# Performance work log

Measured on AMD Instinct MI355X. Metric: run time of the kernel, lower is better.

## Reference

```python
import jax, jax.numpy as jnp
import numpy as np

N_EMBD = 512
BLOCK = 512
HEADS = 16
HEAD_DIM = N_EMBD // HEADS
EPS = 1e-5


def _layernorm(x, g, b):
    mu = jnp.mean(x, axis=-1, keepdims=True)
    var = jnp.mean(jnp.square(x - mu), axis=-1, keepdims=True)
    return (x - mu) * jax.lax.rsqrt(var + EPS) * g + b


def setup_inputs() -> dict:
    key = jax.random.key(0)
    ks = jax.random.split(key, 12)
    B, T, C, H, D = 64, BLOCK, N_EMBD, HEADS, HEAD_DIM
    s = lambda fan_in: 1.0 / np.sqrt(fan_in)
    return {
        "x": jax.random.normal(ks[0], (B, T, C), dtype=jnp.float32),
        # per-head projections, stored (H, C, D) so y = einsum('btc,hcd->bhtd')
        "Wq": jax.random.normal(ks[1], (H, C, D), dtype=jnp.float32) * s(C),
        "Wk": jax.random.normal(ks[2], (H, C, D), dtype=jnp.float32) * s(C),
        "Wv": jax.random.normal(ks[3], (H, C, D), dtype=jnp.float32) * s(C),
        "Wp": jax.random.normal(ks[4], (C, C), dtype=jnp.float32) * s(C),
        "bp": jnp.zeros((C,), dtype=jnp.float32),
        "W1": jax.random.normal(ks[5], (C, 4 * C), dtype=jnp.float32) * s(C),
        "b1": jnp.zeros((4 * C,), dtype=jnp.float32),
        "W2": jax.random.normal(ks[6], (4 * C, C), dtype=jnp.float32) * s(4 * C),
        "b2": jnp.zeros((C,), dtype=jnp.float32),
        "g_ln1": jnp.ones((C,), dtype=jnp.float32),
        "b_ln1": jnp.zeros((C,), dtype=jnp.float32),
        "g_ln2": jnp.ones((C,), dtype=jnp.float32),
        "b_ln2": jnp.zeros((C,), dtype=jnp.float32),
    }


def reference(x, Wq, Wk, Wv, Wp, bp, W1, b1, W2, b2, g_ln1, b_ln1, g_ln2, b_ln2):
    B, T, C = x.shape
    h = _layernorm(x, g_ln1, b_ln1)
    q = jnp.einsum('btc,hcd->bhtd', h, Wq)
    k = jnp.einsum('btc,hcd->bhtd', h, Wk)
    v = jnp.einsum('btc,hcd->bhtd', h, Wv)
    wei = jnp.einsum('bhtd,bhsd->bhts', q, k) * (HEAD_DIM ** -0.5)
    causal = jnp.tril(jnp.ones((T, T), dtype=bool))
    wei = jnp.where(causal, wei, -jnp.inf)
    wei = jax.nn.softmax(wei, axis=-1)  # dropout = identity (eval mode)
    out = jnp.einsum('bhts,bhsd->bhtd', wei, v)
    out = out.transpose(0, 2, 1, 3).reshape(B, T, C)  # concat heads
    sa = out @ Wp + bp
    x = x + sa
    h2 = _layernorm(x, g_ln2, b_ln2)
    ff = jax.nn.relu(h2 @ W1 + b1) @ W2 + b2
    return x + ff
```

## Files before the change

kernel.cpp:

```cpp
#include <hip/hip_runtime.h>
#include <stdint.h>


typedef __attribute__((ext_vector_type(8))) short bf16x8;
typedef __attribute__((ext_vector_type(4))) short bf16x4;
typedef __attribute__((ext_vector_type(4))) float f32x4;

__device__ __forceinline__ unsigned short f2bf(float x) {
  union { float f; unsigned u; } v; v.f = x;
  unsigned r = v.u + 0x7fff + ((v.u >> 16) & 1);
  return (unsigned short)(r >> 16);
}

#if __has_builtin(__builtin_amdgcn_exp2f)
__device__ __forceinline__ float exp2fast(float x) { return __builtin_amdgcn_exp2f(x); }
#else
__device__ __forceinline__ float exp2fast(float x) { return exp2f(x); }
#endif

__device__ __forceinline__ unsigned cvtpk(float lo, float hi) {
  unsigned r; asm("v_cvt_pk_bf16_f32 %0, %1, %2" : "=v"(r) : "v"(lo), "v"(hi)); return r;
}

__device__ __forceinline__ f32x4 MFMA32(bf16x8 a, bf16x8 b, f32x4 c) {
  return __builtin_amdgcn_mfma_f32_16x16x32_bf16(a, b, c, 0, 0, 0);
}

#if __has_builtin(__builtin_amdgcn_mfma_f32_16x16x16bf16_1k)
__device__ __forceinline__ f32x4 MFMA16(bf16x4 a, bf16x4 b, f32x4 c) {
  return __builtin_amdgcn_mfma_f32_16x16x16bf16_1k(a, b, c, 0, 0, 0);
}
#else
__device__ __forceinline__ f32x4 MFMA16(bf16x4 a, bf16x4 b, f32x4 c) {
  f32x4 d;
  asm volatile("v_mfma_f32_16x16x16_bf16 %0, %1, %2, %3\n\ts_nop 7\n\ts_nop 3"
               : "=v"(d) : "v"(a), "v"(b), "v"(c));
  return d;
}
#endif

__device__ __forceinline__ void gload_lds16(const void* g, void* l) {
  __builtin_amdgcn_global_load_lds(
      (const __attribute__((address_space(1))) unsigned int*)(uintptr_t)g,
      (__attribute__((address_space(3))) unsigned int*)(unsigned)(uintptr_t)l,
      16, 0, 0);
}

#define WAITV8() do { asm volatile("s_waitcnt vmcnt(8)" ::: "memory"); } while (0)
#define WAITV0() do { asm volatile("s_waitcnt vmcnt(0)" ::: "memory"); } while (0)
#define WAITL0() do { asm volatile("s_waitcnt lgkmcnt(0)" ::: "memory"); } while (0)
#define SBAR()   __builtin_amdgcn_s_barrier()
#define SCHED0() __builtin_amdgcn_sched_barrier(0)

__global__ __launch_bounds__(256) void prep_qkv_w(
    const float* __restrict__ Wq, const float* __restrict__ Wk,
    const float* __restrict__ Wv, unsigned short* __restrict__ dst)
{
  int idx = blockIdx.x * 256 + threadIdx.x;
  int k = idx & 511;
  int n = idx >> 9;
  int q = n >> 9;
  int hh = (n >> 5) & 15;
  int d = n & 31;
  const float* W = (q == 0) ? Wq : ((q == 1) ? Wk : Wv);
  dst[idx] = f2bf(W[((size_t)hh * 512 + k) * 32 + d]);
}

__global__ __launch_bounds__(256) void transpose_cast(
    const float* __restrict__ src, unsigned short* __restrict__ dst, int Kd, int Nd)
{
  int idx = blockIdx.x * 256 + threadIdx.x;
  int n = idx / Kd, k = idx - n * Kd;
  dst[idx] = f2bf(src[(size_t)k * Nd + n]);
}

__global__ __launch_bounds__(256) void ln_kernel(
    const float* __restrict__ x, const float* __restrict__ g,
    const float* __restrict__ b, unsigned short* __restrict__ out)
{
  const int lane = threadIdx.x & 63;
  const size_t row = (size_t)blockIdx.x * 4 + (threadIdx.x >> 6);
  const float* xp = x + row * 512 + lane * 8;
  float xv[8] __attribute__((aligned(16)));
  *(float4*)(xv)     = *(const float4*)(xp);
  *(float4*)(xv + 4) = *(const float4*)(xp + 4);
  float s = 0.f, s2 = 0.f;
#pragma unroll
  for (int j = 0; j < 8; ++j) { s += xv[j]; s2 += xv[j] * xv[j]; }
#pragma unroll
  for (int m = 1; m < 64; m <<= 1) { s += __shfl_xor(s, m); s2 += __shfl_xor(s2, m); }
  float mean = s * (1.f / 512.f);
  float rstd = rsqrtf(fmaxf(s2 * (1.f / 512.f) - mean * mean, 0.f) + 1e-5f);
  float gv[8] __attribute__((aligned(16))), bv[8] __attribute__((aligned(16)));
  *(float4*)(gv)     = *(const float4*)(g + lane * 8);
  *(float4*)(gv + 4) = *(const float4*)(g + lane * 8 + 4);
  *(float4*)(bv)     = *(const float4*)(b + lane * 8);
  *(float4*)(bv + 4) = *(const float4*)(b + lane * 8 + 4);
  bf16x8 o;
#pragma unroll
  for (int j = 0; j < 8; ++j) o[j] = (short)f2bf((xv[j] - mean) * rstd * gv[j] + bv[j]);
  *(bf16x8*)(out + row * 512 + lane * 8) = o;
}

__global__ __launch_bounds__(256) void vt_kernel(
    const unsigned short* __restrict__ vnat, unsigned short* __restrict__ vt)
{
  __shared__ unsigned short tile[64 * 36];
  const int bh = blockIdx.x >> 3, tt = (blockIdx.x & 7) << 6;
  const int tid = threadIdx.x;
  const int rr = tid >> 2, ch = tid & 3;
  bf16x8 v = *(const bf16x8*)(vnat + ((size_t)bh * 512 + tt + rr) * 32 + ch * 8);
  unsigned short* dst = &tile[rr * 36 + ch * 8];
#pragma unroll
  for (int j = 0; j < 8; ++j) dst[j] = (unsigned short)v[j];
  __syncthreads();
  const int d = tid >> 3, toct = (tid & 7) << 3;
  union { unsigned short s[8]; bf16x8 v8; } o;
#pragma unroll
  for (int j = 0; j < 8; ++j) o.s[j] = tile[(toct + j) * 36 + d];
  *(bf16x8*)(vt + ((size_t)bh * 32 + d) * 512 + tt + toct) = o.v8;
}

template <int MODE>
__device__ __forceinline__ void gemm256_body(
    const unsigned short* __restrict__ A, const unsigned short* __restrict__ Bt,
    int N, int K, int nby,
    unsigned short* __restrict__ obf, float* __restrict__ of32,
    const float* __restrict__ bias, const float* __restrict__ resid,
    unsigned short* __restrict__ vout)
{
  __shared__ __align__(16) unsigned short As[2][256 * 64];
  __shared__ __align__(16) unsigned short Bs[2][256 * 64];
  const int tid = threadIdx.x, lane = tid & 63, wid = tid >> 6;
  const int wr = wid >> 2, wc = wid & 3;
  const int r = lane & 15, hq = lane >> 4;

  const int qq = gridDim.x >> 3;
  const int swz = (blockIdx.x & 7) * qq + (blockIdx.x >> 3);
  const int bx = swz / nby, by = swz - bx * nby;
  const int brow = bx * 256, bcol = by * 256;
  const int nkt = K >> 6;

  const int srow = wid * 32 + (lane >> 3);
  const int schunk = ((lane & 7) ^ ((lane >> 3) & 7)) * 8;
  const unsigned short* Asrc = A + (size_t)(brow + srow) * K + schunk;
  const unsigned short* Bsrc = Bt + (size_t)(bcol + srow) * K + schunk;

  auto STAGE = [&](int t, int buf) {
    const unsigned short* as_ = Asrc + t * 64;
    const unsigned short* bs_ = Bsrc + t * 64;
    char* al_ = (char*)(&As[buf][0]) + wid * 4096;
    char* bl_ = (char*)(&Bs[buf][0]) + wid * 4096;
#pragma unroll
    for (int g = 0; g < 4; ++g) {
      gload_lds16(as_ + (size_t)g * 8 * K, al_ + g * 1024);
      gload_lds16(bs_ + (size_t)g * 8 * K, bl_ + g * 1024);
    }
  };

  const int x0 = ((hq) ^ (r & 7)) * 16;
  const int x1 = ((4 + hq) ^ (r & 7)) * 16;
  const int abase = (wr * 128 + r) * 128;
  const int bbase = (wc * 64 + r) * 128;

  f32x4 acc[8][4] = {};
  bf16x8 af[4][2], bfa[2][2], bfb[2][2];

  STAGE(0, 0);
  STAGE(1, 1);
  WAITV8(); SCHED0();
  SBAR();

  for (int t = 0; t < nkt; ++t) {
    const char* Ab = (const char*)(&As[t & 1][0]);
    const char* Bb = (const char*)(&Bs[t & 1][0]);
#pragma unroll
    for (int m = 0; m < 4; ++m) {
      af[m][0] = *(const bf16x8*)(Ab + abase + m * 2048 + x0);
      af[m][1] = *(const bf16x8*)(Ab + abase + m * 2048 + x1);
    }
#pragma unroll
    for (int n = 0; n < 2; ++n) {
      bfa[n][0] = *(const bf16x8*)(Bb + bbase + n * 2048 + x0);
      bfa[n][1] = *(const bf16x8*)(Bb + bbase + n * 2048 + x1);
    }
    SBAR();
    WAITL0(); SCHED0();
    __builtin_amdgcn_s_setprio(1);
#pragma unroll
    for (int m = 0; m < 4; ++m)
#pragma unroll
      for (int n = 0; n < 2; ++n) {
        acc[m][n] = MFMA32(af[m][0], bfa[n][0], acc[m][n]);
        acc[m][n] = MFMA32(af[m][1], bfa[n][1], acc[m][n]);
      }
    __builtin_amdgcn_s_setprio(0);
    SBAR();
#pragma unroll
    for (int n = 0; n < 2; ++n) {
      bfb[n][0] = *(const bf16x8*)(Bb + bbase + (n + 2) * 2048 + x0);
      bfb[n][1] = *(const bf16x8*)(Bb + bbase + (n + 2) * 2048 + x1);
    }
    SBAR();
    WAITL0(); SCHED0();
    __builtin_amdgcn_s_setprio(1);
#pragma unroll
    for (int m = 0; m < 4; ++m)
#pragma unroll
      for (int n = 0; n < 2; ++n) {
        acc[m][n + 2] = MFMA32(af[m][0], bfb[n][0], acc[m][n + 2]);
        acc[m][n + 2] = MFMA32(af[m][1], bfb[n][1], acc[m][n + 2]);
      }
    __builtin_amdgcn_s_setprio(0);
    SBAR();
#pragma unroll
    for (int m = 0; m < 4; ++m) {
      af[m][0] = *(const bf16x8*)(Ab + abase + 8192 + m * 2048 + x0);
      af[m][1] = *(const bf16x8*)(Ab + abase + 8192 + m * 2048 + x1);
    }
    SBAR();
    WAITL0(); SCHED0();
    __builtin_amdgcn_s_setprio(1);
#pragma unroll
    for (int m = 0; m < 4; ++m)
#pragma unroll
      for (int n = 0; n < 2; ++n) {
        acc[4 + m][n] = MFMA32(af[m][0], bfa[n][0], acc[4 + m][n]);
        acc[4 + m][n] = MFMA32(af[m][1], bfa[n][1], acc[4 + m][n]);
      }
    __builtin_amdgcn_s_setprio(0);
    SBAR();
    if (t + 2 < nkt) STAGE(t + 2, t & 1);
    __builtin_amdgcn_s_setprio(1);
#pragma unroll
    for (int m = 0; m < 4; ++m)
#pragma unroll
      for (int n = 0; n < 2; ++n) {
        acc[4 + m][n + 2] = MFMA32(af[m][0], bfb[n][0], acc[4 + m][n + 2]);
        acc[4 + m][n + 2] = MFMA32(af[m][1], bfb[n][1], acc[4 + m][n + 2]);
      }
    __builtin_amdgcn_s_setprio(0);
    if (t + 2 < nkt) { WAITV8(); } else { WAITV0(); }
    SCHED0();
    SBAR();
  }

#pragma unroll
  for (int m = 0; m < 8; ++m)
#pragma unroll
    for (int n = 0; n < 4; ++n) {
      const int row0 = brow + wr * 128 + m * 16 + hq * 4;
      const int col = bcol + wc * 64 + n * 16 + r;
#pragma unroll
      for (int q2 = 0; q2 < 4; ++q2) {
        const int row = row0 + q2;
        float v = acc[m][n][q2];
        if (MODE == 1) {
          const int which = col >> 9, hh = (col >> 5) & 15, dd = col & 31;
          const int bb = row >> 9, tt = row & 511;
          const size_t off = ((((size_t)bb) * 16 + hh) * 512 + tt) * 32 + dd;
          if (which < 2) {
            if (which == 0) v *= 0.25503521f;
            obf[(size_t)which * 16777216 + off] = f2bf(v);
          } else
            vout[off] = f2bf(v);
        } else if (MODE == 2) {
          v += bias[col] + resid[(size_t)row * N + col];
          of32[(size_t)row * N + col] = v;
        } else if (MODE == 3) {
          v = fmaxf(v + bias[col], 0.f);
          obf[(size_t)row * N + col] = f2bf(v);
        }
      }
    }
}

__global__ __launch_bounds__(512, 2) void qkv_gemm(
    const unsigned short* __restrict__ A, const unsigned short* __restrict__ Bt,
    int N, int K, int nby, unsigned short* __restrict__ obf,
    unsigned short* __restrict__ vout)
{ gemm256_body<1>(A, Bt, N, K, nby, obf, nullptr, nullptr, nullptr, vout); }

__global__ __launch_bounds__(512, 2) void proj_gemm(
    const unsigned short* __restrict__ A, const unsigned short* __restrict__ Bt,
    int N, int K, int nby, float* __restrict__ of32,
    const float* __restrict__ bias, const float* __restrict__ resid)
{ gemm256_body<2>(A, Bt, N, K, nby, nullptr, of32, bias, resid, nullptr); }

__global__ __launch_bounds__(512, 2) void ffn1_gemm(
    const unsigned short* __restrict__ A, const unsigned short* __restrict__ Bt,
    int N, int K, int nby, unsigned short* __restrict__ obf,
    const float* __restrict__ bias)
{ gemm256_body<3>(A, Bt, N, K, nby, obf, nullptr, bias, nullptr, nullptr); }

__global__ __launch_bounds__(512, 2) void ffn2_gemm(
    const unsigned short* __restrict__ A, const unsigned short* __restrict__ Bt,
    int N, int K, int nby, float* __restrict__ of32,
    const float* __restrict__ bias, const float* __restrict__ resid)
{ gemm256_body<2>(A, Bt, N, K, nby, nullptr, of32, bias, resid, nullptr); }

__global__ __launch_bounds__(512, 4) void attn_kernel(
    const unsigned short* __restrict__ Qb, const unsigned short* __restrict__ Kb,
    const unsigned short* __restrict__ Vt, unsigned short* __restrict__ att)
{
  __shared__ __align__(16) unsigned short Ks[512 * 32];
  __shared__ __align__(16) unsigned short Vs[32 * 512];
  const int tid = threadIdx.x, lane = tid & 63, wid = tid >> 6;
  const int bh = blockIdx.x;
  const int r = lane & 15, hq = lane >> 4;
  const unsigned short* Kg = Kb + (size_t)bh * (512 * 32);
  const unsigned short* Vg = Vt + (size_t)bh * (32 * 512);
#pragma unroll
  for (int it = 0; it < 4; ++it) {
    const int c = it * 512 + tid;
    gload_lds16(Kg + c * 8, (char*)Ks + (it * 512 + wid * 64) * 16);
    const int d = c >> 6, sb = c & 63;
    gload_lds16(Vg + d * 512 + (sb ^ (d & 15)) * 8, (char*)Vs + (it * 512 + wid * 64) * 16);
  }
  __syncthreads();

  const f32x4 z = {0.f, 0.f, 0.f, 0.f};
  for (int p = 0; p < 4; ++p) {
    const int t0 = (((p >> 1) << 4) + ((p & 1) ? 15 - wid : wid)) << 4;
    const bf16x8 qf = *(const bf16x8*)(Qb + ((size_t)bh * 512 + t0 + r) * 32 + hq * 8);
    f32x4 o0 = z, o1 = z;
    float m = -1e30f, l = 0.f;
    const int s0m = t0 & ~31;
    for (int s0 = 0; s0 <= s0m; s0 += 32) {
      f32x4 st0 = MFMA32(*(const bf16x8*)((const char*)Ks + (s0 + r) * 64 + hq * 16), qf, z);
      f32x4 st1 = MFMA32(*(const bf16x8*)((const char*)Ks + (s0 + 16 + r) * 64 + hq * 16), qf, z);
      if (s0 == s0m) {
        const int qq = t0 + r;
#pragma unroll
        for (int j = 0; j < 4; ++j) {
          if (s0 + 4 * hq + j > qq)      st0[j] = -1e30f;
          if (s0 + 16 + 4 * hq + j > qq) st1[j] = -1e30f;
        }
      }
      float mx = fmaxf(fmaxf(fmaxf(st0[0], st0[1]), fmaxf(st0[2], st0[3])),
                       fmaxf(fmaxf(st1[0], st1[1]), fmaxf(st1[2], st1[3])));
      mx = fmaxf(mx, __shfl_xor(mx, 16));
      mx = fmaxf(mx, __shfl_xor(mx, 32));
      if (!__all(mx <= m + 8.f)) {
        const float mn = fmaxf(m, mx);
        const float f = exp2fast(m - mn);
        m = mn; l *= f; o0 *= f; o1 *= f;
      }
      float p0[4], p1[4];
#pragma unroll
      for (int j = 0; j < 4; ++j) {
        p0[j] = exp2fast(st0[j] - m);
        p1[j] = exp2fast(st1[j] - m);
      }
      float rs = ((p0[0] + p0[1]) + (p0[2] + p0[3])) + ((p1[0] + p1[1]) + (p1[2] + p1[3]));
      rs += __shfl_xor(rs, 16);
      rs += __shfl_xor(rs, 32);
      l += rs;
      union { unsigned u[2]; bf16x4 v; } a0, a1;
      a0.u[0] = cvtpk(p0[0], p0[1]); a0.u[1] = cvtpk(p0[2], p0[3]);
      a1.u[0] = cvtpk(p1[0], p1[1]); a1.u[1] = cvtpk(p1[2], p1[3]);
      const int lb = (s0 >> 3) + (hq >> 1);
      const char* vb = (const char*)Vs + (hq & 1) * 8;
      o0 = MFMA16(a0.v, *(const bf16x4*)(vb + r * 1024 + ((lb) ^ r) * 16), o0);
      o0 = MFMA16(a1.v, *(const bf16x4*)(vb + r * 1024 + ((lb + 2) ^ r) * 16), o0);
      o1 = MFMA16(a0.v, *(const bf16x4*)(vb + (r + 16) * 1024 + ((lb) ^ r) * 16), o1);
      o1 = MFMA16(a1.v, *(const bf16x4*)(vb + (r + 16) * 1024 + ((lb + 2) ^ r) * 16), o1);
    }
    const size_t ob = ((size_t)(bh >> 4) * 512) * 512 + (size_t)((bh & 15) * 32);
#pragma unroll
    for (int j = 0; j < 4; ++j) {
      const float li = 1.f / __shfl(l, 4 * hq + j);
      const size_t rowb = ob + (size_t)(t0 + 4 * hq + j) * 512;
      att[rowb + r]      = f2bf(o0[j] * li);
      att[rowb + 16 + r] = f2bf(o1[j] * li);
    }
  }
}

extern "C" void kernel_launch(void* const* d_in, const int* in_sizes, int n_in,
                              void* d_out, int out_size, void* d_ws, size_t ws_size,
                              hipStream_t stream)
{
  const float* x   = (const float*)d_in[0];
  const float* Wq  = (const float*)d_in[1];
  const float* Wk  = (const float*)d_in[2];
  const float* Wv  = (const float*)d_in[3];
  const float* Wp  = (const float*)d_in[4];
  const float* bp  = (const float*)d_in[5];
  const float* W1  = (const float*)d_in[6];
  const float* b1  = (const float*)d_in[7];
  const float* W2  = (const float*)d_in[8];
  const float* b2  = (const float*)d_in[9];
  const float* g1  = (const float*)d_in[10];
  const float* bb1 = (const float*)d_in[11];
  const float* g2  = (const float*)d_in[12];
  const float* bb2 = (const float*)d_in[13];
  float* out = (float*)d_out;

  char* ws = (char*)d_ws;
  unsigned short* h    = (unsigned short*)(ws);
  unsigned short* wqkv = (unsigned short*)(ws + 33554432);
  unsigned short* wp   = (unsigned short*)(ws + 35127296);
  unsigned short* w1   = (unsigned short*)(ws + 35651584);
  unsigned short* w2   = (unsigned short*)(ws + 37748736);
  unsigned short* qk   = (unsigned short*)(ws + 39845888);
  unsigned short* vt   = qk + (size_t)2 * 16777216;
  unsigned short* att  = vt + 16777216;
  unsigned short* vnat = att;
  unsigned short* mid  = qk;
  if (ws_size < 174063616) return;

  prep_qkv_w<<<3072, 256, 0, stream>>>(Wq, Wk, Wv, wqkv);
  transpose_cast<<<1024, 256, 0, stream>>>(Wp, wp, 512, 512);
  transpose_cast<<<4096, 256, 0, stream>>>(W1, w1, 512, 2048);
  transpose_cast<<<4096, 256, 0, stream>>>(W2, w2, 2048, 512);

  ln_kernel<<<8192, 256, 0, stream>>>(x, g1, bb1, h);

  qkv_gemm<<<768, 512, 0, stream>>>(h, wqkv, 1536, 512, 6, qk, vnat);

  vt_kernel<<<8192, 256, 0, stream>>>(vnat, vt);

  attn_kernel<<<1024, 512, 0, stream>>>(qk, qk + 16777216, vt, att);

  proj_gemm<<<256, 512, 0, stream>>>(att, wp, 512, 512, 2, out, bp, x);

  ln_kernel<<<8192, 256, 0, stream>>>(out, g2, bb2, h);

  ffn1_gemm<<<1024, 512, 0, stream>>>(h, w1, 2048, 512, 8, mid, b1);

  ffn2_gemm<<<256, 512, 0, stream>>>(mid, w2, 512, 2048, 2, out, b2, out);
}
```

Baseline: 418.7 us.

## Tile weight transpose-casts through LDS and split GEMM A/B staging with fewer barriers

The weight prep kernels now go through shared-memory 64x64 tiles with vectorized float4 loads and bf16x8 stores, replacing the old one-element-per-thread strided gathers. The shared GEMM main loop splits staging into separate A and B loads. It issues the B prefetch earlier, before the third MFMA phase, and drops three barriers per k-iteration. The intent is to cut uncoalesced weight-prep traffic and reduce synchronisation stalls in the GEMMs. The risk is that early overwriting of the Bs buffer could race with other waves' reads, since those barriers were removed.

```diff
diff --git a/kernel.cpp b/kernel.cpp
--- a/kernel.cpp
+++ b/kernel.cpp
@@ -56,22 +56,51 @@
     const float* __restrict__ Wq, const float* __restrict__ Wk,
     const float* __restrict__ Wv, unsigned short* __restrict__ dst)
 {
-  int idx = blockIdx.x * 256 + threadIdx.x;
-  int k = idx & 511;
-  int n = idx >> 9;
-  int q = n >> 9;
-  int hh = (n >> 5) & 15;
-  int d = n & 31;
+  __shared__ float tile[64 * 33];
+  const int b = blockIdx.x;
+  const int q = b / 128, hh = (b >> 3) & 15, kt = (b & 7) << 6;
   const float* W = (q == 0) ? Wq : ((q == 1) ? Wk : Wv);
-  dst[idx] = f2bf(W[((size_t)hh * 512 + k) * 32 + d]);
+  const int t = threadIdx.x;
+  const int rr = t >> 2, ch = (t & 3) << 3;
+  const float* sp = W + ((size_t)hh * 512 + kt + rr) * 32 + ch;
+  float4 v0 = *(const float4*)(sp), v1 = *(const float4*)(sp + 4);
+  float* dp = &tile[rr * 33 + ch];
+  dp[0] = v0.x; dp[1] = v0.y; dp[2] = v0.z; dp[3] = v0.w;
+  dp[4] = v1.x; dp[5] = v1.y; dp[6] = v1.z; dp[7] = v1.w;
+  __syncthreads();
+  const int d = t >> 3, toct = (t & 7) << 3;
+  bf16x8 o;
+#pragma unroll
+  for (int j = 0; j < 8; ++j) o[j] = (short)f2bf(tile[(toct + j) * 33 + d]);
+  *(bf16x8*)(dst + ((size_t)q * 512 + hh * 32 + d) * 512 + kt + toct) = o;
 }
 
 __global__ __launch_bounds__(256) void transpose_cast(
     const float* __restrict__ src, unsigned short* __restrict__ dst, int Kd, int Nd)
 {
-  int idx = blockIdx.x * 256 + threadIdx.x;
-  int n = idx / Kd, k = idx - n * Kd;
-  dst[idx] = f2bf(src[(size_t)k * Nd + n]);
+  __shared__ float tile[64 * 65];
+  const int nk = Kd >> 6;
+  const int kt = (blockIdx.x % nk) << 6, nt = (blockIdx.x / nk) << 6;
+  const int t = threadIdx.x;
+  const int rr = t >> 2, ch = (t & 3) << 4;
+  const float* sp = src + (size_t)(kt + rr) * Nd + nt + ch;
+  float* dp = &tile[rr * 65 + ch];
+#pragma unroll
+  for (int c = 0; c < 4; ++c) {
+    float4 v = *(const float4*)(sp + c * 4);
+    dp[c * 4 + 0] = v.x; dp[c * 4 + 1] = v.y; dp[c * 4 + 2] = v.z; dp[c * 4 + 3] = v.w;
+  }
+  __syncthreads();
+  const int nn = t >> 2, c2 = (t & 3) << 4;
+  bf16x8 o0, o1;
+#pragma unroll
+  for (int j = 0; j < 8; ++j) {
+    o0[j] = (short)f2bf(tile[(c2 + j) * 65 + nn]);
+    o1[j] = (short)f2bf(tile[(c2 + 8 + j) * 65 + nn]);
+  }
+  unsigned short* op = dst + (size_t)(nt + nn) * Kd + kt + c2;
+  *(bf16x8*)(op) = o0;
+  *(bf16x8*)(op + 8) = o1;
 }
 
 __global__ __launch_bounds__(256) void ln_kernel(
@@ -146,16 +175,17 @@
   const unsigned short* Asrc = A + (size_t)(brow + srow) * K + schunk;
   const unsigned short* Bsrc = Bt + (size_t)(bcol + srow) * K + schunk;
 
-  auto STAGE = [&](int t, int buf) {
+  auto STAGE_A = [&](int t, int buf) {
     const unsigned short* as_ = Asrc + t * 64;
+    char* al_ = (char*)(&As[buf][0]) + wid * 4096;
+#pragma unroll
+    for (int g = 0; g < 4; ++g) gload_lds16(as_ + (size_t)g * 8 * K, al_ + g * 1024);
+  };
+  auto STAGE_B = [&](int t, int buf) {
     const unsigned short* bs_ = Bsrc + t * 64;
-    char* al_ = (char*)(&As[buf][0]) + wid * 4096;
     char* bl_ = (char*)(&Bs[buf][0]) + wid * 4096;
 #pragma unroll
-    for (int g = 0; g < 4; ++g) {
-      gload_lds16(as_ + (size_t)g * 8 * K, al_ + g * 1024);
-      gload_lds16(bs_ + (size_t)g * 8 * K, bl_ + g * 1024);
-    }
+    for (int g = 0; g < 4; ++g) gload_lds16(bs_ + (size_t)g * 8 * K, bl_ + g * 1024);
   };
 
   const int x0 = ((hq) ^ (r & 7)) * 16;
@@ -166,8 +196,8 @@
   f32x4 acc[8][4] = {};
   bf16x8 af[4][2], bfa[2][2], bfb[2][2];
 
-  STAGE(0, 0);
-  STAGE(1, 1);
+  STAGE_A(0, 0); STAGE_B(0, 0);
+  STAGE_A(1, 1); STAGE_B(1, 1);
   WAITV8(); SCHED0();
   SBAR();
 
@@ -184,7 +214,6 @@
       bfa[n][0] = *(const bf16x8*)(Bb + bbase + n * 2048 + x0);
       bfa[n][1] = *(const bf16x8*)(Bb + bbase + n * 2048 + x1);
     }
-    SBAR();
     WAITL0(); SCHED0();
     __builtin_amdgcn_s_setprio(1);
 #pragma unroll
@@ -201,7 +230,6 @@
       bfb[n][0] = *(const bf16x8*)(Bb + bbase + (n + 2) * 2048 + x0);
       bfb[n][1] = *(const bf16x8*)(Bb + bbase + (n + 2) * 2048 + x1);
     }
-    SBAR();
     WAITL0(); SCHED0();
     __builtin_amdgcn_s_setprio(1);
 #pragma unroll
@@ -218,7 +246,7 @@
       af[m][0] = *(const bf16x8*)(Ab + abase + 8192 + m * 2048 + x0);
       af[m][1] = *(const bf16x8*)(Ab + abase + 8192 + m * 2048 + x1);
     }
-    SBAR();
+    if (t + 2 < nkt) STAGE_B(t + 2, t & 1);
     WAITL0(); SCHED0();
     __builtin_amdgcn_s_setprio(1);
 #pragma unroll
@@ -230,7 +258,7 @@
       }
     __builtin_amdgcn_s_setprio(0);
     SBAR();
-    if (t + 2 < nkt) STAGE(t + 2, t & 1);
+    if (t + 2 < nkt) STAGE_A(t + 2, t & 1);
     __builtin_amdgcn_s_setprio(1);
 #pragma unroll
     for (int m = 0; m < 4; ++m)
@@ -410,10 +438,10 @@
   unsigned short* mid  = qk;
   if (ws_size < 174063616) return;
 
-  prep_qkv_w<<<3072, 256, 0, stream>>>(Wq, Wk, Wv, wqkv);
-  transpose_cast<<<1024, 256, 0, stream>>>(Wp, wp, 512, 512);
-  transpose_cast<<<4096, 256, 0, stream>>>(W1, w1, 512, 2048);
-  transpose_cast<<<4096, 256, 0, stream>>>(W2, w2, 2048, 512);
+  prep_qkv_w<<<384, 256, 0, stream>>>(Wq, Wk, Wv, wqkv);
+  transpose_cast<<<64, 256, 0, stream>>>(Wp, wp, 512, 512);
+  transpose_cast<<<256, 256, 0, stream>>>(W1, w1, 512, 2048);
+  transpose_cast<<<256, 256, 0, stream>>>(W2, w2, 2048, 512);
 
   ln_kernel<<<8192, 256, 0, stream>>>(x, g1, bb1, h);
 
```

Result: faster. 390.8 us (-6.7%).
